# Kernel tuning notes

Measured on AMD Instinct MI355X. Metric: run time of the kernel, lower is better.

Reference implementation:

```python
import jax, jax.numpy as jnp
import numpy as np

SQRT2 = 1.4142135623730951  # lrelu def_gain
LRELU_SLOPE = 0.2
EPS = 1e-8


def setup_inputs() -> dict:
    key = jax.random.key(0)
    k1, k2, k3, k4 = jax.random.split(key, 4)
    B, C_in, C_out, H, W, K, DLAT = 8, 512, 512, 32, 32, 3, 512
    x = jax.random.normal(k1, (B, C_in, H, W), dtype=jnp.float32)
    y = jax.random.normal(k2, (B, DLAT), dtype=jnp.float32)
    # init_std = 1.0 since use_wscale=True, lrmul=1
    weight = jax.random.normal(k3, (C_out, C_in, K, K), dtype=jnp.float32)
    mod_weight = jax.random.normal(k4, (C_in, DLAT), dtype=jnp.float32)
    bias = jnp.ones((C_in,), dtype=jnp.float32)
    return {"x": x, "y": y, "weight": weight, "mod_weight": mod_weight, "bias": bias}


def reference(x, y, weight, mod_weight, bias):
    B, C_in, H, W = x.shape
    C_out, _, K, _ = weight.shape
    dlat = mod_weight.shape[1]
    w_mul_mod = dlat ** (-0.5)  # EqualizedLinear wscale; conv w_mul is unused in forward
    # style: s = sqrt(2) * lrelu(y @ W_mod^T + b)
    s = y @ (mod_weight * w_mul_mod).T  # [B, C_in]
    s = jax.nn.leaky_relu(s + bias, LRELU_SLOPE) * SQRT2
    # modulate per-sample weights: [B, C_out, C_in, K, K]
    ww = weight[None] * s[:, None, :, None, None]
    # demodulate
    d = jax.lax.rsqrt(jnp.sum(ww * ww, axis=(2, 3, 4)) + EPS)  # [B, C_out]
    ww = ww * d[:, :, None, None, None]
    # fused grouped conv: groups = batch
    xg = x.reshape(1, B * C_in, H, W)
    wg = ww.reshape(B * C_out, C_in, K, K)
    out = jax.lax.conv_general_dilated(
        xg, wg, window_strides=(1, 1), padding="SAME",
        dimension_numbers=("NCHW", "OIHW", "NCHW"),
        feature_group_count=B)
    return out.reshape(B, C_out, H, W)
```

## Files before the change

kernel.cpp:

```cpp
#include <hip/hip_runtime.h>
#include <hip/hip_bf16.h>

typedef float f32x4 __attribute__((ext_vector_type(4)));
typedef short bf16x8 __attribute__((ext_vector_type(8)));

#define LRELU_SLOPE 0.2f
#define SQRT2F 1.4142135623730951f
#define MODSCALE 0.044194173824159216f

#define GLL(SRC, DST)                                                       \
  __builtin_amdgcn_global_load_lds(                                         \
      (const __attribute__((address_space(1))) unsigned int*)(SRC),         \
      (__attribute__((address_space(3))) unsigned int*)(DST), 16, 0, 0)

__global__ __launch_bounds__(64) void style_kernel(const float* __restrict__ y,
                                                   const float* __restrict__ mw,
                                                   const float* __restrict__ bias,
                                                   float* __restrict__ s) {
  int ci = blockIdx.x;
  int l = threadIdx.x;
  const float4* mwr = reinterpret_cast<const float4*>(mw + ci * 512);
  float4 m0 = mwr[2 * l], m1 = mwr[2 * l + 1];
  float acc[8];
#pragma unroll
  for (int b = 0; b < 8; ++b) {
    const float4* yr = reinterpret_cast<const float4*>(y + b * 512);
    float4 y0 = yr[2 * l], y1 = yr[2 * l + 1];
    acc[b] = m0.x * y0.x + m0.y * y0.y + m0.z * y0.z + m0.w * y0.w +
             m1.x * y1.x + m1.y * y1.y + m1.z * y1.z + m1.w * y1.w;
  }
#pragma unroll
  for (int off = 32; off > 0; off >>= 1) {
#pragma unroll
    for (int b = 0; b < 8; ++b) acc[b] += __shfl_xor(acc[b], off, 64);
  }
  if (l < 8) {
    float v = acc[l] * MODSCALE + bias[ci];
    v = v > 0.f ? v : LRELU_SLOPE * v;
    s[l * 512 + ci] = v * SQRT2F;
  }
}

__global__ __launch_bounds__(256) void wprep_kernel(const float* __restrict__ w,
                                                    __hip_bfloat16* __restrict__ wt,
                                                    float* __restrict__ wsq) {
  int idx = blockIdx.x * 256 + threadIdx.x;
  const float* p = w + (size_t)idx * 9;
  float v[9];
  float sq = 0.f;
#pragma unroll
  for (int t = 0; t < 9; ++t) {
    v[t] = p[t];
    sq += v[t] * v[t];
  }
  wsq[idx] = sq;
#pragma unroll
  for (int t = 0; t < 9; ++t) wt[t * 262144 + idx] = __float2bfloat16(v[t]);
}

__global__ __launch_bounds__(64) void demod_kernel(const float* __restrict__ wsq,
                                                   const float* __restrict__ s,
                                                   float* __restrict__ d) {
  int co = blockIdx.x;
  int l = threadIdx.x;
  const float4* qr = reinterpret_cast<const float4*>(wsq + co * 512);
  float4 q0 = qr[2 * l], q1 = qr[2 * l + 1];
  float acc[8];
#pragma unroll
  for (int b = 0; b < 8; ++b) {
    const float4* sr = reinterpret_cast<const float4*>(s + b * 512);
    float4 s0 = sr[2 * l], s1 = sr[2 * l + 1];
    acc[b] = q0.x * s0.x * s0.x + q0.y * s0.y * s0.y + q0.z * s0.z * s0.z +
             q0.w * s0.w * s0.w + q1.x * s1.x * s1.x + q1.y * s1.y * s1.y +
             q1.z * s1.z * s1.z + q1.w * s1.w * s1.w;
  }
#pragma unroll
  for (int off = 32; off > 0; off >>= 1) {
#pragma unroll
    for (int b = 0; b < 8; ++b) acc[b] += __shfl_xor(acc[b], off, 64);
  }
  if (l < 8) d[l * 512 + co] = rsqrtf(acc[l] + 1e-8f);
}

__global__ __launch_bounds__(256) void xs_kernel(const float* __restrict__ x,
                                                 const float* __restrict__ s,
                                                 __hip_bfloat16* __restrict__ xsp) {
  int bid = blockIdx.x;
  int cc = bid & 7;
  int h = (bid >> 3) & 31;
  int b = bid >> 8;
  int tid = threadIdx.x;
  __shared__ __hip_bfloat16 tile[32][72];

  int cil = tid >> 2;
  int w0 = (tid & 3) * 8;
  int ci = cc * 64 + cil;
  const float* xp = x + (((size_t)(b * 512 + ci) * 32 + h) << 5) + w0;
  float sv = s[b * 512 + ci];
  float4 a0 = *reinterpret_cast<const float4*>(xp);
  float4 a1 = *reinterpret_cast<const float4*>(xp + 4);
  tile[w0 + 0][cil] = __float2bfloat16(a0.x * sv);
  tile[w0 + 1][cil] = __float2bfloat16(a0.y * sv);
  tile[w0 + 2][cil] = __float2bfloat16(a0.z * sv);
  tile[w0 + 3][cil] = __float2bfloat16(a0.w * sv);
  tile[w0 + 4][cil] = __float2bfloat16(a1.x * sv);
  tile[w0 + 5][cil] = __float2bfloat16(a1.y * sv);
  tile[w0 + 6][cil] = __float2bfloat16(a1.z * sv);
  tile[w0 + 7][cil] = __float2bfloat16(a1.w * sv);
  __syncthreads();

  int wloc = tid >> 3;
  int cj = (tid & 7) * 8;
  int4 v = *reinterpret_cast<const int4*>(&tile[wloc][cj]);
  unsigned off = (unsigned)((b * 34 + h + 1) * 34 + (wloc + 1)) * 512 + cc * 64 + cj;
  *reinterpret_cast<int4*>(xsp + off) = v;
}

__global__ __launch_bounds__(512, 2) void conv_kernel(const __hip_bfloat16* __restrict__ xsp,
                                                      const __hip_bfloat16* __restrict__ wt,
                                                      const float* __restrict__ dmod,
                                                      float* __restrict__ out) {
  __shared__ __hip_bfloat16 As_[2][256 * 64];
  __shared__ __hip_bfloat16 Bs_[3][128 * 64];
  const int bid = blockIdx.x;
  const int xcd = bid & 7, slot = bid >> 3;
  const int bm = xcd * 8 + (slot >> 2);
  const int bn = slot & 3;
  const int tid = threadIdx.x;
  const int wv = tid >> 6;
  const int l = tid & 63;
  const int kg = wv >> 2;
  const int wr = (wv >> 1) & 1, wc = wv & 1;
  const int bb = bm >> 3;
  const int h0 = (bm & 7) << 2;

  const int swz = (((l & 7) ^ (l >> 3)) << 3);
  unsigned boff[2];
#pragma unroll
  for (int j = 0; j < 2; ++j) {
    int row = ((j * 8 + wv) << 3) + (l >> 3);
    boff[j] = (unsigned)((bn << 7) + row) * 512 + swz;
  }
  unsigned ahoff[4];
#pragma unroll
  for (int j = 0; j < 4; ++j) {
    int r = j * 64 + wv * 8 + (l >> 3);
    int rc = r > 203 ? 203 : r;
    int hr = rc / 34, hc = rc - hr * 34;
    ahoff[j] = (unsigned)((bb * 34 + h0 + hr) * 34 + hc) * 512 + swz;
  }
  int pb[4];
#pragma unroll
  for (int m = 0; m < 4; ++m)
    pb[m] = ((wr << 1) + (m >> 1)) * 34 + ((m & 1) << 4) + (l & 15);

  f32x4 acc[4][4];
#pragma unroll
  for (int n = 0; n < 4; ++n)
#pragma unroll
    for (int m = 0; m < 4; ++m) acc[n][m] = (f32x4)0.f;

  auto stageB = [&](__hip_bfloat16* Bn, int t, int k0c) {
    const __hip_bfloat16* src = wt + t * 262144 + k0c * 64;
#pragma unroll
    for (int j = 0; j < 2; ++j)
      GLL(src + boff[j], Bn + ((j * 8 + wv) << 9));
  };
  auto stageA1 = [&](__hip_bfloat16* An, int j, int kn) {
    GLL(xsp + ahoff[j] + kn * 64, An + ((j * 64 + wv * 8) << 6));
  };
  auto phase = [&](const __hip_bfloat16* Aq, const __hip_bfloat16* Bq, int dh, int dw) {
    const int cb = (kg << 2) + (l >> 4);
    bf16x8 af[4], bfr[4];
#pragma unroll
    for (int m = 0; m < 4; ++m) {
      int p = pb[m] + dh * 34 + dw;
      af[m] = *reinterpret_cast<const bf16x8*>(Aq + p * 64 + ((cb ^ (p & 7)) << 3));
    }
#pragma unroll
    for (int n = 0; n < 4; ++n) {
      int row = (wc << 6) + (n << 4) + (l & 15);
      bfr[n] = *reinterpret_cast<const bf16x8*>(Bq + row * 64 + ((cb ^ (l & 7)) << 3));
    }
#pragma unroll
    for (int n = 0; n < 4; ++n)
#pragma unroll
      for (int m = 0; m < 4; ++m)
        acc[n][m] = __builtin_amdgcn_mfma_f32_16x16x32_bf16(bfr[n], af[m], acc[n][m], 0, 0, 0);
  };

#define SB0 __builtin_amdgcn_sched_barrier(0)
#define WAITBAR(N)                                          \
  asm volatile("s_waitcnt vmcnt(" #N ")" ::: "memory");     \
  __builtin_amdgcn_s_barrier();                             \
  SB0

#pragma unroll
  for (int j = 0; j < 4; ++j) stageA1(&As_[0][0], j, 0);
  SB0;
  stageB(&Bs_[0][0], 0, 0);
  stageB(&Bs_[1][0], 1, 0);

#pragma unroll 1
  for (int k0 = 0; k0 < 7; ++k0) {
    const __hip_bfloat16* Aq = &As_[k0 & 1][0];
    __hip_bfloat16* An = &As_[(k0 + 1) & 1][0];
    WAITBAR(2); stageB(&Bs_[2][0], 2, k0); SB0; stageA1(An, 0, k0 + 1); SB0;
    phase(Aq, &Bs_[0][0], 0, 0);
    WAITBAR(3); stageB(&Bs_[0][0], 3, k0); SB0; stageA1(An, 1, k0 + 1); SB0;
    phase(Aq, &Bs_[1][0], 0, 1);
    WAITBAR(4); stageB(&Bs_[1][0], 4, k0); SB0; stageA1(An, 2, k0 + 1); SB0;
    phase(Aq, &Bs_[2][0], 0, 2);
    WAITBAR(4); stageB(&Bs_[2][0], 5, k0); SB0; stageA1(An, 3, k0 + 1); SB0;
    phase(Aq, &Bs_[0][0], 1, 0);
    WAITBAR(4); stageB(&Bs_[0][0], 6, k0); SB0;
    phase(Aq, &Bs_[1][0], 1, 1);
    WAITBAR(3); stageB(&Bs_[1][0], 7, k0); SB0;
    phase(Aq, &Bs_[2][0], 1, 2);
    WAITBAR(2); stageB(&Bs_[2][0], 8, k0); SB0;
    phase(Aq, &Bs_[0][0], 2, 0);
    WAITBAR(2); stageB(&Bs_[0][0], 0, k0 + 1); SB0;
    phase(Aq, &Bs_[1][0], 2, 1);
    WAITBAR(2); stageB(&Bs_[1][0], 1, k0 + 1); SB0;
    phase(Aq, &Bs_[2][0], 2, 2);
  }
  {
    const __hip_bfloat16* Aq = &As_[1][0];
    WAITBAR(2); stageB(&Bs_[2][0], 2, 7); SB0; phase(Aq, &Bs_[0][0], 0, 0);
    WAITBAR(2); stageB(&Bs_[0][0], 3, 7); SB0; phase(Aq, &Bs_[1][0], 0, 1);
    WAITBAR(2); stageB(&Bs_[1][0], 4, 7); SB0; phase(Aq, &Bs_[2][0], 0, 2);
    WAITBAR(2); stageB(&Bs_[2][0], 5, 7); SB0; phase(Aq, &Bs_[0][0], 1, 0);
    WAITBAR(2); stageB(&Bs_[0][0], 6, 7); SB0; phase(Aq, &Bs_[1][0], 1, 1);
    WAITBAR(2); stageB(&Bs_[1][0], 7, 7); SB0; phase(Aq, &Bs_[2][0], 1, 2);
    WAITBAR(2); stageB(&Bs_[2][0], 8, 7); SB0; phase(Aq, &Bs_[0][0], 2, 0);
    WAITBAR(2); phase(Aq, &Bs_[1][0], 2, 1);
    WAITBAR(0); phase(Aq, &Bs_[2][0], 2, 2);
  }
#undef WAITBAR
#undef SB0

  float* red = reinterpret_cast<float*>(&As_[0][0]);
  __syncthreads();
  if (kg == 1) {
#pragma unroll
    for (int n = 0; n < 4; ++n)
#pragma unroll
      for (int m = 0; m < 4; ++m)
        *reinterpret_cast<f32x4*>(red + (n * 4 + m) * 1024 + (wv & 3) * 256 + l * 4) =
            acc[n][m];
  }
  __syncthreads();
  if (kg == 0) {
    const int pixbase = ((bm & 7) << 7) + (wr << 6) + (l & 15);
    const int cob = (bn << 7) + (wc << 6) + ((l >> 4) << 2);
    float* ob = out + ((size_t)bb << 19);
    const float* drow = dmod + bb * 512;
#pragma unroll
    for (int n = 0; n < 4; ++n) {
#pragma unroll
      for (int m = 0; m < 4; ++m)
        acc[n][m] += *reinterpret_cast<const f32x4*>(red + (n * 4 + m) * 1024 + wv * 256 + l * 4);
#pragma unroll
      for (int jj = 0; jj < 4; ++jj) {
        const int co = cob + (n << 4) + jj;
        const float dv = drow[co];
        float* orow = ob + ((unsigned)co << 10) + pixbase;
#pragma unroll
        for (int m = 0; m < 4; ++m) orow[m << 4] = acc[n][m][jj] * dv;
      }
    }
  }
}

extern "C" void kernel_launch(void* const* d_in, const int* in_sizes, int n_in,
                              void* d_out, int out_size, void* d_ws, size_t ws_size,
                              hipStream_t stream) {
  (void)in_sizes; (void)n_in; (void)out_size; (void)ws_size;
  const float* x = (const float*)d_in[0];
  const float* y = (const float*)d_in[1];
  const float* w = (const float*)d_in[2];
  const float* mw = (const float*)d_in[3];
  const float* bias = (const float*)d_in[4];
  float* out = (float*)d_out;

  char* ws = (char*)d_ws;
  float* s = (float*)(ws + 0);
  float* dmod = (float*)(ws + 16384);
  float* wsq = (float*)(ws + 32768);
  __hip_bfloat16* wt = (__hip_bfloat16*)(ws + 1081344);
  __hip_bfloat16* xsp = (__hip_bfloat16*)(ws + 5799936);

  hipMemsetAsync(xsp, 0, 9469952, stream);
  style_kernel<<<512, 64, 0, stream>>>(y, mw, bias, s);
  wprep_kernel<<<1024, 256, 0, stream>>>(w, wt, wsq);
  demod_kernel<<<512, 64, 0, stream>>>(wsq, s, dmod);
  xs_kernel<<<2048, 256, 0, stream>>>(x, s, xsp);
  conv_kernel<<<256, 512, 0, stream>>>(xsp, wt, dmod, out);
}
```

Before: 68.48 us.

## Stage weight taps in groups of three with double-buffered B and MFMA priority

Restructures the conv main loop so weight tiles are loaded three taps at a time into two 3-tap buffers. This gives three barriers per K-chunk instead of nine, each followed by three MFMA phases. The A tile shrinks to 224 rows, and the last staging group uses only half the waves. The epilogue reduction buffer moves to Bs_, and s_setprio is raised around the MFMA blocks. The goal is to cut barrier and waitcnt overhead, at the cost of more LDS and full vmcnt(0) waits that may expose load latency.

```diff
diff --git a/kernel.cpp b/kernel.cpp
--- a/kernel.cpp
+++ b/kernel.cpp
@@ -120,8 +120,8 @@
                                                       const __hip_bfloat16* __restrict__ wt,
                                                       const float* __restrict__ dmod,
                                                       float* __restrict__ out) {
-  __shared__ __hip_bfloat16 As_[2][256 * 64];
-  __shared__ __hip_bfloat16 Bs_[3][128 * 64];
+  __shared__ __hip_bfloat16 As_[2][224 * 64];
+  __shared__ __hip_bfloat16 Bs_[2][3 * 128 * 64];
   const int bid = blockIdx.x;
   const int xcd = bid & 7, slot = bid >> 3;
   const int bm = xcd * 8 + (slot >> 2);
@@ -142,12 +142,15 @@
     boff[j] = (unsigned)((bn << 7) + row) * 512 + swz;
   }
   unsigned ahoff[4];
+  int adst[4];
 #pragma unroll
   for (int j = 0; j < 4; ++j) {
-    int r = j * 64 + wv * 8 + (l >> 3);
+    int rb = j < 3 ? j * 64 + wv * 8 : 192 + (wv & 3) * 8;
+    int r = rb + (l >> 3);
     int rc = r > 203 ? 203 : r;
     int hr = rc / 34, hc = rc - hr * 34;
-    ahoff[j] = (unsigned)((bb * 34 + h0 + hr) * 34 + hc) * 512 + swz;
+    ahoff[j] = (unsigned)((bb * 34 + h0 + hr) * 34 + hc) * 512 + (((l & 7) ^ (r & 7)) << 3);
+    adst[j] = rb;
   }
   int pb[4];
 #pragma unroll
@@ -167,7 +170,7 @@
       GLL(src + boff[j], Bn + ((j * 8 + wv) << 9));
   };
   auto stageA1 = [&](__hip_bfloat16* An, int j, int kn) {
-    GLL(xsp + ahoff[j] + kn * 64, An + ((j * 64 + wv * 8) << 6));
+    GLL(xsp + ahoff[j] + kn * 64, An + (adst[j] << 6));
   };
   auto phase = [&](const __hip_bfloat16* Aq, const __hip_bfloat16* Bq, int dh, int dw) {
     const int cb = (kg << 2) + (l >> 4);
@@ -182,64 +185,68 @@
       int row = (wc << 6) + (n << 4) + (l & 15);
       bfr[n] = *reinterpret_cast<const bf16x8*>(Bq + row * 64 + ((cb ^ (l & 7)) << 3));
     }
+    __builtin_amdgcn_s_setprio(1);
 #pragma unroll
     for (int n = 0; n < 4; ++n)
 #pragma unroll
       for (int m = 0; m < 4; ++m)
         acc[n][m] = __builtin_amdgcn_mfma_f32_16x16x32_bf16(bfr[n], af[m], acc[n][m], 0, 0, 0);
+    __builtin_amdgcn_s_setprio(0);
   };
 
 #define SB0 __builtin_amdgcn_sched_barrier(0)
-#define WAITBAR(N)                                          \
-  asm volatile("s_waitcnt vmcnt(" #N ")" ::: "memory");     \
+#define WAITBAR0                                            \
+  asm volatile("s_waitcnt vmcnt(0)" ::: "memory");          \
   __builtin_amdgcn_s_barrier();                             \
   SB0
 
 #pragma unroll
   for (int j = 0; j < 4; ++j) stageA1(&As_[0][0], j, 0);
   SB0;
-  stageB(&Bs_[0][0], 0, 0);
-  stageB(&Bs_[1][0], 1, 0);
+  stageB(&Bs_[0][0] + 0 * 8192, 0, 0);
+  stageB(&Bs_[0][0] + 1 * 8192, 1, 0);
+  stageB(&Bs_[0][0] + 2 * 8192, 2, 0);
 
 #pragma unroll 1
-  for (int k0 = 0; k0 < 7; ++k0) {
+  for (int k0 = 0; k0 < 8; ++k0) {
     const __hip_bfloat16* Aq = &As_[k0 & 1][0];
     __hip_bfloat16* An = &As_[(k0 + 1) & 1][0];
-    WAITBAR(2); stageB(&Bs_[2][0], 2, k0); SB0; stageA1(An, 0, k0 + 1); SB0;
-    phase(Aq, &Bs_[0][0], 0, 0);
-    WAITBAR(3); stageB(&Bs_[0][0], 3, k0); SB0; stageA1(An, 1, k0 + 1); SB0;
-    phase(Aq, &Bs_[1][0], 0, 1);
-    WAITBAR(4); stageB(&Bs_[1][0], 4, k0); SB0; stageA1(An, 2, k0 + 1); SB0;
-    phase(Aq, &Bs_[2][0], 0, 2);
-    WAITBAR(4); stageB(&Bs_[2][0], 5, k0); SB0; stageA1(An, 3, k0 + 1); SB0;
-    phase(Aq, &Bs_[0][0], 1, 0);
-    WAITBAR(4); stageB(&Bs_[0][0], 6, k0); SB0;
-    phase(Aq, &Bs_[1][0], 1, 1);
-    WAITBAR(3); stageB(&Bs_[1][0], 7, k0); SB0;
-    phase(Aq, &Bs_[2][0], 1, 2);
-    WAITBAR(2); stageB(&Bs_[2][0], 8, k0); SB0;
-    phase(Aq, &Bs_[0][0], 2, 0);
-    WAITBAR(2); stageB(&Bs_[0][0], 0, k0 + 1); SB0;
-    phase(Aq, &Bs_[1][0], 2, 1);
-    WAITBAR(2); stageB(&Bs_[1][0], 1, k0 + 1); SB0;
-    phase(Aq, &Bs_[2][0], 2, 2);
-  }
-  {
-    const __hip_bfloat16* Aq = &As_[1][0];
-    WAITBAR(2); stageB(&Bs_[2][0], 2, 7); SB0; phase(Aq, &Bs_[0][0], 0, 0);
-    WAITBAR(2); stageB(&Bs_[0][0], 3, 7); SB0; phase(Aq, &Bs_[1][0], 0, 1);
-    WAITBAR(2); stageB(&Bs_[1][0], 4, 7); SB0; phase(Aq, &Bs_[2][0], 0, 2);
-    WAITBAR(2); stageB(&Bs_[2][0], 5, 7); SB0; phase(Aq, &Bs_[0][0], 1, 0);
-    WAITBAR(2); stageB(&Bs_[0][0], 6, 7); SB0; phase(Aq, &Bs_[1][0], 1, 1);
-    WAITBAR(2); stageB(&Bs_[1][0], 7, 7); SB0; phase(Aq, &Bs_[2][0], 1, 2);
-    WAITBAR(2); stageB(&Bs_[2][0], 8, 7); SB0; phase(Aq, &Bs_[0][0], 2, 0);
-    WAITBAR(2); phase(Aq, &Bs_[1][0], 2, 1);
-    WAITBAR(0); phase(Aq, &Bs_[2][0], 2, 2);
-  }
-#undef WAITBAR
+    __hip_bfloat16* Br = &Bs_[k0 & 1][0];
+    __hip_bfloat16* Bo = &Bs_[(k0 & 1) ^ 1][0];
+    const int kn = k0 + 1;
+    WAITBAR0;
+    stageB(Bo + 0 * 8192, 3, k0);
+    stageB(Bo + 1 * 8192, 4, k0);
+    stageB(Bo + 2 * 8192, 5, k0);
+    if (k0 < 7) { stageA1(An, 0, kn); stageA1(An, 1, kn); }
+    SB0;
+    phase(Aq, Br + 0 * 8192, 0, 0);
+    phase(Aq, Br + 1 * 8192, 0, 1);
+    phase(Aq, Br + 2 * 8192, 0, 2);
+    WAITBAR0;
+    stageB(Br + 0 * 8192, 6, k0);
+    stageB(Br + 1 * 8192, 7, k0);
+    stageB(Br + 2 * 8192, 8, k0);
+    if (k0 < 7) { stageA1(An, 2, kn); stageA1(An, 3, kn); }
+    SB0;
+    phase(Aq, Bo + 0 * 8192, 1, 0);
+    phase(Aq, Bo + 1 * 8192, 1, 1);
+    phase(Aq, Bo + 2 * 8192, 1, 2);
+    WAITBAR0;
+    if (k0 < 7) {
+      stageB(Bo + 0 * 8192, 0, kn);
+      stageB(Bo + 1 * 8192, 1, kn);
+      stageB(Bo + 2 * 8192, 2, kn);
+    }
+    SB0;
+    phase(Aq, Br + 0 * 8192, 2, 0);
+    phase(Aq, Br + 1 * 8192, 2, 1);
+    phase(Aq, Br + 2 * 8192, 2, 2);
+  }
+#undef WAITBAR0
 #undef SB0
 
-  float* red = reinterpret_cast<float*>(&As_[0][0]);
+  float* red = reinterpret_cast<float*>(&Bs_[0][0]);
   __syncthreads();
   if (kg == 1) {
 #pragma unroll
```

Result: slower. 70.22 us (+2.6%).
